# Kernel optimization log

Hardware: AMD Instinct MI355X
Metric: run time of the kernel (lower is better)

The kernel has to match this reference:

```python
import jax, jax.numpy as jnp
import numpy as np
import math

B = 16          # graphs per batch
N = 2048        # nodes per graph
F_IN = 64       # input node features
E_PER = 32768   # edges per graph
E = B * E_PER
H = 128         # hidden width (fixed by module)
C = 10          # output classes
K = math.ceil(0.8 * N)  # TopKPooling keep count per graph = 1639


def setup_inputs() -> dict:
    key = jax.random.key(0)
    ks = jax.random.split(key, 24)
    x = jax.random.normal(ks[0], (B * N, F_IN), jnp.float32)
    # intra-graph random edges (source->target), global node ids
    gid = jnp.repeat(jnp.arange(B, dtype=jnp.int32), E_PER)
    src = gid * N + jax.random.randint(ks[1], (E,), 0, N, dtype=jnp.int32)
    dst = gid * N + jax.random.randint(ks[2], (E,), 0, N, dtype=jnp.int32)

    def lin_w(k, o, i):
        return jax.random.normal(k, (o, i), jnp.float32) / jnp.sqrt(i)

    inp = dict(x=x, src=src, dst=dst)
    # GraphConv: lin_rel (with bias) on aggregated neighbors + lin_root (no bias)
    inp.update(W1_rel=lin_w(ks[3], H, F_IN), b1=jnp.zeros((H,), jnp.float32), W1_root=lin_w(ks[4], H, F_IN))
    inp.update(W2_rel=lin_w(ks[5], H, H), b2=jnp.zeros((H,), jnp.float32), W2_root=lin_w(ks[6], H, H))
    inp.update(W3_rel=lin_w(ks[7], H, H), b3=jnp.zeros((H,), jnp.float32), W3_root=lin_w(ks[8], H, H))
    inp.update(pool_w=jax.random.normal(ks[9], (H,), jnp.float32) / jnp.sqrt(H))
    inp.update(Wl1=lin_w(ks[10], 128, 256), bl1=jnp.zeros((128,), jnp.float32))
    inp.update(Wl2=lin_w(ks[11], 64, 128), bl2=jnp.zeros((64,), jnp.float32))
    inp.update(Wl3=lin_w(ks[12], C, 64), bl3=jnp.zeros((C,), jnp.float32))
    return inp


def _graph_conv(x, src, dst, W_rel, b, W_root, n_nodes, emask=None):
    # out_i = W_rel @ (sum_{j->i} x_j) + b + W_root @ x_i
    msg = x[src]
    if emask is not None:
        msg = msg * emask[:, None]
    agg = jax.ops.segment_sum(msg, dst, num_segments=n_nodes)
    return agg @ W_rel.T + b + x @ W_root.T


def _global_pools(x, n_per_graph):
    xb = x.reshape(B, n_per_graph, -1)
    return jnp.concatenate([xb.max(axis=1), xb.mean(axis=1)], axis=1)  # [B, 2F]


def reference(x, src, dst, W1_rel, b1, W1_root, W2_rel, b2, W2_root,
              W3_rel, b3, W3_root, pool_w, Wl1, bl1, Wl2, bl2, Wl3, bl3):
    n0 = B * N
    h = jax.nn.relu(_graph_conv(x, src, dst, W1_rel, b1, W1_root, n0))
    x1 = _global_pools(h, N)

    h = jax.nn.relu(_graph_conv(h, src, dst, W2_rel, b2, W2_root, n0))

    # TopKPooling(ratio=0.8): score = tanh(x@w/||w||); keep top-k per graph;
    # kept features scaled by score; edges with a dropped endpoint removed.
    score = jnp.tanh((h @ pool_w) / jnp.linalg.norm(pool_w))  # [B*N]
    top_s, top_i = jax.lax.top_k(score.reshape(B, N), K)      # [B,K]
    perm = (top_i + jnp.arange(B)[:, None] * N).reshape(-1)   # global old ids [B*K]
    h = h[perm] * top_s.reshape(-1)[:, None]                  # [B*K, H]

    n1 = B * K
    new_id = jnp.full((n0,), -1, jnp.int32).at[perm].set(jnp.arange(n1, dtype=jnp.int32))
    ns, nd = new_id[src], new_id[dst]
    keep = ((ns >= 0) & (nd >= 0)).astype(h.dtype)
    ns = jnp.where(ns >= 0, ns, 0)
    nd = jnp.where(nd >= 0, nd, 0)

    x2 = _global_pools(h, K)
    h = jax.nn.relu(_graph_conv(h, ns, nd, W3_rel, b3, W3_root, n1, emask=keep))
    x3 = _global_pools(h, K)

    z = x1 + x2 + x3
    z = jax.nn.relu(z @ Wl1.T + bl1)
    z = jax.nn.relu(z @ Wl2.T + bl2)
    return jax.nn.log_softmax(z @ Wl3.T + bl3, axis=-1)  # [B, C]
```

## Files before the change

kernel.cpp:

```cpp
#include <hip/hip_runtime.h>
#include <hip/hip_bf16.h>
#include <math.h>

#define NB 32768
#define NN 2048
#define BG 16
#define KK 1639
#define KKP 1664
#define N1 (BG*KK)
#define N1P (BG*KKP)
#define EE 524288
#define HH 128
#define FIN 64

using half8 = __attribute__((ext_vector_type(8))) _Float16;
using half4 = __attribute__((ext_vector_type(4))) _Float16;
using f32x4 = __attribute__((ext_vector_type(4))) float;

__device__ __forceinline__ void acc4(f32x4& a, const float4& v) {
  a[0] += v.x; a[1] += v.y; a[2] += v.z; a[3] += v.w;
}

__global__ void deg_kernel(const int* __restrict__ dst, int* deg, int n) {
  int e = blockIdx.x * blockDim.x + threadIdx.x;
  if (e < n) atomicAdd(&deg[dst[e]], 1);
}

__global__ void exscan_kernel(const int* __restrict__ deg, int* rs, int* cursor, int n) {
  __shared__ int wsum[16];
  __shared__ int carry;
  int t = threadIdx.x;
  int lane = t & 63, wid = t >> 6;
  if (t == 0) carry = 0;
  __syncthreads();
  int ntiles = (n + 4095) >> 12;
  for (int tile = 0; tile < ntiles; ++tile) {
    int idx = (tile << 12) + t * 4;
    int4 v4 = *(const int4*)(deg + idx);
    int v0 = (idx + 0 < n) ? v4.x : 0;
    int v1 = (idx + 1 < n) ? v4.y : 0;
    int v2 = (idx + 2 < n) ? v4.z : 0;
    int v3 = (idx + 3 < n) ? v4.w : 0;
    int s = v0 + v1 + v2 + v3;
    int pre = s;
#pragma unroll
    for (int off = 1; off < 64; off <<= 1) {
      int u = __shfl_up(pre, off, 64);
      if (lane >= off) pre += u;
    }
    if (lane == 63) wsum[wid] = pre;
    __syncthreads();
    int wbase = 0;
#pragma unroll
    for (int ww = 0; ww < 16; ++ww)
      if (ww < wid) wbase += wsum[ww];
    int ex = carry + wbase + (pre - s);
    int4 e4 = make_int4(ex, ex + v0, ex + v0 + v1, ex + v0 + v1 + v2);
    if (idx + 3 < n) {
      *(int4*)(rs + idx) = e4;
      *(int4*)(cursor + idx) = e4;
    } else {
      if (idx + 0 < n) { rs[idx + 0] = e4.x; cursor[idx + 0] = e4.x; }
      if (idx + 1 < n) { rs[idx + 1] = e4.y; cursor[idx + 1] = e4.y; }
      if (idx + 2 < n) { rs[idx + 2] = e4.z; cursor[idx + 2] = e4.z; }
    }
    int tot = 0;
    if (t == 1023) tot = ex + s;
    __syncthreads();
    if (t == 1023) carry = tot;
    __syncthreads();
  }
  if (t == 0) rs[n] = carry;
}

__global__ void scatter_kernel(const int* __restrict__ src, const int* __restrict__ dst,
                               int* cursor, int* csr, int n) {
  int e = blockIdx.x * blockDim.x + threadIdx.x;
  if (e < n) {
    int d = dst[e];
    int p = atomicAdd(&cursor[d], 1);
    csr[p] = src[e];
  }
}

template <int KD1, int KD2, int POOL, int SCORE, int REMAP>
__global__ __launch_bounds__(512, 4) void conv_mfma(
    const float* __restrict__ feat, const float* __restrict__ xr,
    const int* __restrict__ rs, const int* __restrict__ csr,
    const int* __restrict__ perm, const int* __restrict__ new_id,
    const _Float16* __restrict__ Wh, const _Float16* __restrict__ Wl,
    const float* __restrict__ bias, float* __restrict__ out, int M, int nwg,
    float* __restrict__ pmax, float* __restrict__ psum,
    const float* __restrict__ pw, float* __restrict__ score) {
  constexpr int KTOT = KD1 + KD2;
  constexpr int NSTEP = KTOT / 32;
  __shared__ _Float16 ah_lds[64 * KTOT];
  __shared__ _Float16 al_lds[64 * KTOT];
  __shared__ float sdot[64][8];
  __shared__ float swsq[8];

  int tid = threadIdx.x;
  int lane = tid & 63, wid = tid >> 6;
  int bq = nwg >> 3, br = nwg & 7, bx = blockIdx.x & 7, bi = blockIdx.x >> 3;
  int swz = (bx < br ? bx * (bq + 1) : br * (bq + 1) + (bx - br) * bq) + bi;
  int row0 = swz * 64;
  int ch0 = wid * 16;
  int col = lane & 15;
  int kseg = (lane >> 4) * 8;

  {
    constexpr int CH = KD1 / 4;
    constexpr int EPW = 64 / CH;
    int sub = lane / CH;
    int ch = lane % CH;
    const float4* feat4 = (const float4*)feat;
#pragma unroll
    for (int rr = 0; rr < 8; ++rr) {
      int gr = wid * 8 + rr;
      int grow = row0 + gr;
      int e0 = 0, e1 = 0;
      if (REMAP) {
        int g = grow / KKP, j = grow - g * KKP;
        if (j < KK) {
          int oldrow = perm[g * KK + j];
          e0 = rs[oldrow];
          e1 = rs[oldrow + 1];
        }
      } else {
        if (grow >= M) grow = M - 1;
        e0 = rs[grow];
        e1 = rs[grow + 1];
      }
      f32x4 a0 = {0.f, 0.f, 0.f, 0.f}, a1 = a0, a2 = a0, a3 = a0;
      int e = e0 + sub;
      for (; e + 7 * EPW < e1; e += 8 * EPW) {
        int c[8];
#pragma unroll
        for (int u = 0; u < 8; ++u) c[u] = csr[e + u * EPW];
        if (REMAP) {
#pragma unroll
          for (int u = 0; u < 8; ++u) c[u] = new_id[c[u]];
        }
        float4 v[8];
#pragma unroll
        for (int u = 0; u < 8; ++u) {
          int ci = (REMAP && c[u] < 0) ? 0 : c[u];
          v[u] = feat4[(size_t)ci * CH + ch];
        }
        if (REMAP) {
#pragma unroll
          for (int u = 0; u < 8; ++u)
            if (c[u] < 0) v[u] = make_float4(0.f, 0.f, 0.f, 0.f);
        }
        acc4(a0, v[0]); acc4(a1, v[1]); acc4(a2, v[2]); acc4(a3, v[3]);
        acc4(a0, v[4]); acc4(a1, v[5]); acc4(a2, v[6]); acc4(a3, v[7]);
      }
      for (; e + 3 * EPW < e1; e += 4 * EPW) {
        int c[4];
#pragma unroll
        for (int u = 0; u < 4; ++u) c[u] = csr[e + u * EPW];
        if (REMAP) {
#pragma unroll
          for (int u = 0; u < 4; ++u) c[u] = new_id[c[u]];
        }
        float4 v[4];
#pragma unroll
        for (int u = 0; u < 4; ++u) {
          int ci = (REMAP && c[u] < 0) ? 0 : c[u];
          v[u] = feat4[(size_t)ci * CH + ch];
        }
        if (REMAP) {
#pragma unroll
          for (int u = 0; u < 4; ++u)
            if (c[u] < 0) v[u] = make_float4(0.f, 0.f, 0.f, 0.f);
        }
        acc4(a0, v[0]); acc4(a1, v[1]); acc4(a2, v[2]); acc4(a3, v[3]);
      }
      for (; e < e1; e += EPW) {
        int c = csr[e];
        if (REMAP) {
          c = new_id[c];
          if (c < 0) continue;
        }
        float4 v = feat4[(size_t)c * CH + ch];
        acc4(a0, v);
      }
      f32x4 s = (a0 + a1) + (a2 + a3);
      if (EPW == 4) {
#pragma unroll
        for (int j = 0; j < 4; ++j) s[j] += __shfl_xor(s[j], 16, 64);
      }
      if (EPW >= 2) {
#pragma unroll
        for (int j = 0; j < 4; ++j) s[j] += __shfl_xor(s[j], 32, 64);
      }
      if (sub == 0) {
        half4 hi, lo;
#pragma unroll
        for (int j = 0; j < 4; ++j) {
          _Float16 h = (_Float16)s[j];
          hi[j] = h;
          lo[j] = (_Float16)(s[j] - (float)h);
        }
        int byte = ((gr * KTOT + ch * 4) * 2) ^ ((gr & 7) << 4);
        *(half4*)((char*)ah_lds + byte) = hi;
        *(half4*)((char*)al_lds + byte) = lo;
      }
    }
  }

  for (int idx = tid; idx < 64 * KD2 / 8; idx += 512) {
    int row = idx / (KD2 / 8);
    int kc = (idx % (KD2 / 8)) * 8;
    int grow = row0 + row;
    if (grow >= M) grow = M - 1;
    const float* sp = xr + (size_t)grow * KD2 + kc;
    float4 a0 = *(const float4*)sp;
    float4 a1 = *(const float4*)(sp + 4);
    float av[8] = {a0.x, a0.y, a0.z, a0.w, a1.x, a1.y, a1.z, a1.w};
    half8 vh, vl;
#pragma unroll
    for (int j = 0; j < 8; ++j) {
      _Float16 h = (_Float16)av[j];
      vh[j] = h;
      vl[j] = (_Float16)(av[j] - (float)h);
    }
    int byte = ((row * KTOT + KD1 + kc) * 2) ^ ((row & 7) << 4);
    *(half8*)((char*)ah_lds + byte) = vh;
    *(half8*)((char*)al_lds + byte) = vl;
  }

  size_t wbase = (size_t)(ch0 + col) * KTOT + kseg;
  half8 whc = *(const half8*)(Wh + wbase);
  half8 wlc = *(const half8*)(Wl + wbase);
  __syncthreads();

  f32x4 acc[4];
#pragma unroll
  for (int rf = 0; rf < 4; ++rf) acc[rf] = (f32x4){0.f, 0.f, 0.f, 0.f};
  int r = lane & 15;
#pragma unroll
  for (int s = 0; s < NSTEP; ++s) {
    half8 whn, wln;
    if (s + 1 < NSTEP) {
      whn = *(const half8*)(Wh + wbase + (s + 1) * 32);
      wln = *(const half8*)(Wl + wbase + (s + 1) * 32);
    }
#pragma unroll
    for (int rf = 0; rf < 4; ++rf) {
      int row = rf * 16 + r;
      int byte = ((row * KTOT + s * 32 + kseg) * 2) ^ ((row & 7) << 4);
      half8 a_h = *(const half8*)((const char*)ah_lds + byte);
      half8 a_l = *(const half8*)((const char*)al_lds + byte);
      acc[rf] = __builtin_amdgcn_mfma_f32_16x16x32_f16(a_l, whc, acc[rf], 0, 0, 0);
      acc[rf] = __builtin_amdgcn_mfma_f32_16x16x32_f16(a_h, wlc, acc[rf], 0, 0, 0);
      acc[rf] = __builtin_amdgcn_mfma_f32_16x16x32_f16(a_h, whc, acc[rf], 0, 0, 0);
    }
    if (s + 1 < NSTEP) { whc = whn; wlc = wln; }
  }

  float bv = bias[ch0 + col];
  float cmax = -3.402823466e38f, csum = 0.f;
  float wcol = SCORE ? pw[ch0 + col] : 0.f;
  float pd[4][4];
  int g = 0, rowbase = 0;
  if (POOL == 2) { g = row0 / KKP; rowbase = row0 - g * KKP; }
#pragma unroll
  for (int rf = 0; rf < 4; ++rf) {
    int orow0 = row0 + rf * 16 + (lane >> 4) * 4;
#pragma unroll
    for (int rr = 0; rr < 4; ++rr) {
      int orow = orow0 + rr;
      float v = fmaxf(acc[rf][rr] + bv, 0.f);
      if (orow < M) out[(size_t)orow * HH + ch0 + col] = v;
      if (POOL == 1) { cmax = fmaxf(cmax, v); csum += v; }
      if (POOL == 2) {
        int local = rowbase + rf * 16 + (lane >> 4) * 4 + rr;
        if (local < KK) { cmax = fmaxf(cmax, v); csum += v; }
      }
      if (SCORE) pd[rf][rr] = v * wcol;
    }
  }
  if (POOL) {
    cmax = fmaxf(cmax, __shfl_xor(cmax, 16, 64)); csum += __shfl_xor(csum, 16, 64);
    cmax = fmaxf(cmax, __shfl_xor(cmax, 32, 64)); csum += __shfl_xor(csum, 32, 64);
    if ((lane >> 4) == 0) {
      if (POOL == 1) {
        int gg = row0 >> 11, sb = (row0 & 2047) >> 6;
        pmax[(gg * 32 + sb) * HH + ch0 + col] = cmax;
        psum[(gg * 32 + sb) * HH + ch0 + col] = csum;
      } else {
        int sb = rowbase >> 6;
        pmax[(g * 26 + sb) * HH + ch0 + col] = cmax;
        psum[(g * 26 + sb) * HH + ch0 + col] = csum;
      }
    }
  }
  if (SCORE) {
#pragma unroll
    for (int rf = 0; rf < 4; ++rf)
#pragma unroll
      for (int rr = 0; rr < 4; ++rr) {
        float d = pd[rf][rr];
        d += __shfl_xor(d, 1, 64); d += __shfl_xor(d, 2, 64);
        d += __shfl_xor(d, 4, 64); d += __shfl_xor(d, 8, 64);
        if (col == 0) sdot[rf * 16 + (lane >> 4) * 4 + rr][wid] = d;
      }
    float wsq = wcol * wcol;
    wsq += __shfl_xor(wsq, 1, 64); wsq += __shfl_xor(wsq, 2, 64);
    wsq += __shfl_xor(wsq, 4, 64); wsq += __shfl_xor(wsq, 8, 64);
    if (lane == 0) swsq[wid] = wsq;
    __syncthreads();
    if (tid < 64) {
      float d = 0.f, q = 0.f;
#pragma unroll
      for (int wv = 0; wv < 8; ++wv) { d += sdot[tid][wv]; q += swsq[wv]; }
      score[row0 + tid] = tanhf(d * rsqrtf(q));
    }
  }
}

__global__ void prep_weights_f16(const float* __restrict__ W1_rel, const float* __restrict__ W1_root,
                                 const float* __restrict__ W2_rel, const float* __restrict__ W2_root,
                                 const float* __restrict__ W3_rel, const float* __restrict__ W3_root,
                                 _Float16* wh1, _Float16* wl1, _Float16* wh2, _Float16* wl2,
                                 _Float16* wh3, _Float16* wl3) {
  int idx = blockIdx.x * blockDim.x + threadIdx.x;
  float v;
  _Float16* ph;
  _Float16* pl;
  int j;
  if (idx < 128 * 128) {
    j = idx;
    int o = j >> 7, k = j & 127;
    v = (k < 64) ? W1_rel[o * 64 + k] : W1_root[o * 64 + (k - 64)];
    ph = wh1; pl = wl1;
  } else if (idx < 128 * 128 + 128 * 256) {
    j = idx - 128 * 128;
    int o = j >> 8, k = j & 255;
    v = (k < 128) ? W2_rel[o * 128 + k] : W2_root[o * 128 + (k - 128)];
    ph = wh2; pl = wl2;
  } else if (idx < 128 * 128 + 2 * 128 * 256) {
    j = idx - 128 * 128 - 128 * 256;
    int o = j >> 8, k = j & 255;
    v = (k < 128) ? W3_rel[o * 128 + k] : W3_root[o * 128 + (k - 128)];
    ph = wh3; pl = wl3;
  } else {
    return;
  }
  _Float16 h = (_Float16)v;
  ph[j] = h;
  pl[j] = (_Float16)(v - (float)h);
}

__global__ void topk_kernel(const float* __restrict__ score, int* perm) {
  __shared__ unsigned long long k[NN];
  int b = blockIdx.x;
  int tid = threadIdx.x;
  for (int i = tid; i < NN; i += 1024) {
    float s = score[b * NN + i];
    unsigned u = __float_as_uint(s);
    u = (u & 0x80000000u) ? ~u : (u | 0x80000000u);
    unsigned long long key = ((unsigned long long)u << 32) | (unsigned)(NN - 1 - i);
    k[i] = ~key;
  }
  __syncthreads();
  for (int kk = 2; kk <= NN; kk <<= 1) {
    for (int j = kk >> 1; j > 0; j >>= 1) {
      for (int t = tid; t < NN; t += 1024) {
        int ixj = t ^ j;
        if (ixj > t) {
          bool up = ((t & kk) == 0);
          unsigned long long a = k[t], c = k[ixj];
          if ((a > c) == up) { k[t] = c; k[ixj] = a; }
        }
      }
      __syncthreads();
    }
  }
  for (int j = tid; j < KK; j += 1024) {
    unsigned long long key = ~k[j];
    int i = (NN - 1) - (int)(key & 0xffffffffu);
    perm[b * KK + j] = b * NN + i;
  }
}

__global__ void h3_kernel(const float4* __restrict__ h2, const int* __restrict__ perm,
                          const float* __restrict__ score, float4* __restrict__ h3,
                          int* __restrict__ new_id) {
  int idx = blockIdx.x * blockDim.x + threadIdx.x;
  if (idx < N1 * 32) {
    int g = idx >> 5, c = idx & 31;
    int b = g / KK, j = g - b * KK;
    int p = perm[g];
    if (c == 0) new_id[p] = b * KKP + j;
    float s = score[p];
    float4 v = h2[(size_t)p * 32 + c];
    v.x *= s; v.y *= s; v.z *= s; v.w *= s;
    h3[(size_t)(b * KKP + j) * 32 + c] = v;
  }
}

__global__ void pool2_kernel(const float* __restrict__ h, float* pmax, float* psum) {
  int b = blockIdx.x / 26, s = blockIdx.x % 26;
  int f = threadIdx.x;
  int r0 = s * 64, r1 = min(KK, r0 + 64);
  float m = -3.402823466e38f, sum = 0.f;
  for (int r = r0; r < r1; ++r) {
    float v = h[(size_t)(b * KKP + r) * HH + f];
    m = fmaxf(m, v);
    sum += v;
  }
  pmax[(b * 26 + s) * HH + f] = m;
  psum[(b * 26 + s) * HH + f] = sum;
}

__global__ void mlp_kernel(const float* __restrict__ pm1, const float* __restrict__ ps1,
                           const float* __restrict__ pm2, const float* __restrict__ ps2,
                           const float* __restrict__ pm3, const float* __restrict__ ps3,
                           const float* __restrict__ Wl1, const float* __restrict__ bl1,
                           const float* __restrict__ Wl2, const float* __restrict__ bl2,
                           const float* __restrict__ Wl3, const float* __restrict__ bl3,
                           float* out) {
  __shared__ float z[256], a1[128], a2[64], a3[10], red[2];
  int b = blockIdx.x, t = threadIdx.x;
  float m1 = -3.402823466e38f, m2 = m1, m3 = m1;
  float s1 = 0.f, s2 = 0.f, s3 = 0.f;
  for (int s = 0; s < 32; ++s) {
    int o = (b * 32 + s) * 128 + t;
    m1 = fmaxf(m1, pm1[o]); s1 += ps1[o];
  }
  for (int s = 0; s < 26; ++s) {
    int o = (b * 26 + s) * 128 + t;
    m2 = fmaxf(m2, pm2[o]); s2 += ps2[o];
    m3 = fmaxf(m3, pm3[o]); s3 += ps3[o];
  }
  z[t] = m1 + m2 + m3;
  z[128 + t] = s1 * (1.f / NN) + (s2 + s3) * (1.f / KK);
  __syncthreads();
  {
    float acc = bl1[t];
    for (int q = 0; q < 256; ++q) acc = fmaf(Wl1[t * 256 + q], z[q], acc);
    a1[t] = fmaxf(acc, 0.f);
  }
  __syncthreads();
  if (t < 64) {
    float acc = bl2[t];
    for (int q = 0; q < 128; ++q) acc = fmaf(Wl2[t * 128 + q], a1[q], acc);
    a2[t] = fmaxf(acc, 0.f);
  }
  __syncthreads();
  if (t < 10) {
    float acc = bl3[t];
    for (int q = 0; q < 64; ++q) acc = fmaf(Wl3[t * 64 + q], a2[q], acc);
    a3[t] = acc;
  }
  __syncthreads();
  if (t == 0) {
    float m = a3[0];
    for (int i = 1; i < 10; ++i) m = fmaxf(m, a3[i]);
    float s = 0.f;
    for (int i = 0; i < 10; ++i) s += expf(a3[i] - m);
    red[0] = m;
    red[1] = logf(s);
  }
  __syncthreads();
  if (t < 10) out[b * 10 + t] = a3[t] - red[0] - red[1];
}

extern "C" void kernel_launch(void* const* d_in, const int* in_sizes, int n_in,
                              void* d_out, int out_size, void* d_ws, size_t ws_size,
                              hipStream_t stream) {
  const float* x       = (const float*)d_in[0];
  const int*   src     = (const int*)d_in[1];
  const int*   dst     = (const int*)d_in[2];
  const float* W1_rel  = (const float*)d_in[3];
  const float* b1      = (const float*)d_in[4];
  const float* W1_root = (const float*)d_in[5];
  const float* W2_rel  = (const float*)d_in[6];
  const float* b2      = (const float*)d_in[7];
  const float* W2_root = (const float*)d_in[8];
  const float* W3_rel  = (const float*)d_in[9];
  const float* b3      = (const float*)d_in[10];
  const float* W3_root = (const float*)d_in[11];
  const float* pool_w  = (const float*)d_in[12];
  const float* Wl1     = (const float*)d_in[13];
  const float* bl1     = (const float*)d_in[14];
  const float* Wl2     = (const float*)d_in[15];
  const float* bl2     = (const float*)d_in[16];
  const float* Wl3     = (const float*)d_in[17];
  const float* bl3     = (const float*)d_in[18];
  float* out = (float*)d_out;

  char* w = (char*)d_ws;
  size_t off = 0;
  auto alloc = [&](size_t bytes) -> char* {
    off = (off + 255) & ~(size_t)255;
    char* p = w + off;
    off += bytes;
    return p;
  };
  int* deg1     = (int*)alloc((NB + 4096) * 4);
  int* rs1      = (int*)alloc((NB + 1) * 4);
  int* cursor1  = (int*)alloc(NB * 4);
  int* csr1     = (int*)alloc((size_t)EE * 4);
  int* new_id   = (int*)alloc(NB * 4);
  int* perm     = (int*)alloc(N1 * 4);
  _Float16* wh1 = (_Float16*)alloc(128 * 128 * 2);
  _Float16* wl1 = (_Float16*)alloc(128 * 128 * 2);
  _Float16* wh2 = (_Float16*)alloc(128 * 256 * 2);
  _Float16* wl2 = (_Float16*)alloc(128 * 256 * 2);
  _Float16* wh3 = (_Float16*)alloc(128 * 256 * 2);
  _Float16* wl3 = (_Float16*)alloc(128 * 256 * 2);
  float* bufA   = (float*)alloc((size_t)NB * HH * 4);
  float* bufB   = (float*)alloc((size_t)NB * HH * 4);
  float* score  = (float*)alloc(NB * 4);
  float* pm1    = (float*)alloc(BG * 32 * HH * 4);
  float* ps1    = (float*)alloc(BG * 32 * HH * 4);
  float* pm2    = (float*)alloc(BG * 26 * HH * 4);
  float* ps2    = (float*)alloc(BG * 26 * HH * 4);
  float* pm3    = (float*)alloc(BG * 26 * HH * 4);
  float* ps3    = (float*)alloc(BG * 26 * HH * 4);
  if (off > ws_size) return;

  const int TB = 256;
  const int egrid = (EE + TB - 1) / TB;

  hipMemsetAsync(deg1, 0, (NB + 4096) * 4, stream);
  hipMemsetAsync(new_id, 0xFF, NB * 4, stream);

  prep_weights_f16<<<(128 * 128 + 2 * 128 * 256 + TB - 1) / TB, TB, 0, stream>>>(
      W1_rel, W1_root, W2_rel, W2_root, W3_rel, W3_root, wh1, wl1, wh2, wl2, wh3, wl3);

  deg_kernel<<<egrid, TB, 0, stream>>>(dst, deg1, EE);
  exscan_kernel<<<1, 1024, 0, stream>>>(deg1, rs1, cursor1, NB);
  scatter_kernel<<<egrid, TB, 0, stream>>>(src, dst, cursor1, csr1, EE);

  conv_mfma<64, 64, 1, 0, 0><<<NB / 64, 512, 0, stream>>>(
      x, x, rs1, csr1, nullptr, nullptr, wh1, wl1, b1, bufA, NB, NB / 64, pm1, ps1,
      nullptr, nullptr);

  conv_mfma<128, 128, 0, 1, 0><<<NB / 64, 512, 0, stream>>>(
      bufA, bufA, rs1, csr1, nullptr, nullptr, wh2, wl2, b2, bufB, NB, NB / 64,
      nullptr, nullptr, pool_w, score);

  topk_kernel<<<BG, 1024, 0, stream>>>(score, perm);
  h3_kernel<<<(N1 * 32 + TB - 1) / TB, TB, 0, stream>>>((const float4*)bufB, perm, score,
                                                        (float4*)bufA, new_id);
  pool2_kernel<<<BG * 26, 128, 0, stream>>>(bufA, pm2, ps2);

  conv_mfma<128, 128, 2, 0, 1><<<N1P / 64, 512, 0, stream>>>(
      bufA, bufA, rs1, csr1, perm, new_id, wh3, wl3, b3, bufB, N1P, N1P / 64, pm3, ps3,
      nullptr, nullptr);

  mlp_kernel<<<BG, 128, 0, stream>>>(pm1, ps1, pm2, ps2, pm3, ps3,
                                     Wl1, bl1, Wl2, bl2, Wl3, bl3, out);
}
```

Before: 239.0 us.

## Halve conv row tile to 32 and replace bitonic top-k with radix select

```diff
diff --git a/kernel.cpp b/kernel.cpp
--- a/kernel.cpp
+++ b/kernel.cpp
@@ -94,16 +94,16 @@
     const float* __restrict__ pw, float* __restrict__ score) {
   constexpr int KTOT = KD1 + KD2;
   constexpr int NSTEP = KTOT / 32;
-  __shared__ _Float16 ah_lds[64 * KTOT];
-  __shared__ _Float16 al_lds[64 * KTOT];
-  __shared__ float sdot[64][8];
+  __shared__ _Float16 ah_lds[32 * KTOT];
+  __shared__ _Float16 al_lds[32 * KTOT];
+  __shared__ float sdot[32][8];
   __shared__ float swsq[8];
 
   int tid = threadIdx.x;
   int lane = tid & 63, wid = tid >> 6;
   int bq = nwg >> 3, br = nwg & 7, bx = blockIdx.x & 7, bi = blockIdx.x >> 3;
   int swz = (bx < br ? bx * (bq + 1) : br * (bq + 1) + (bx - br) * bq) + bi;
-  int row0 = swz * 64;
+  int row0 = swz * 32;
   int ch0 = wid * 16;
   int col = lane & 15;
   int kseg = (lane >> 4) * 8;
@@ -115,8 +115,8 @@
     int ch = lane % CH;
     const float4* feat4 = (const float4*)feat;
 #pragma unroll
-    for (int rr = 0; rr < 8; ++rr) {
-      int gr = wid * 8 + rr;
+    for (int rr = 0; rr < 4; ++rr) {
+      int gr = wid * 4 + rr;
       int grow = row0 + gr;
       int e0 = 0, e1 = 0;
       if (REMAP) {
@@ -190,10 +190,8 @@
 #pragma unroll
         for (int j = 0; j < 4; ++j) s[j] += __shfl_xor(s[j], 16, 64);
       }
-      if (EPW >= 2) {
-#pragma unroll
-        for (int j = 0; j < 4; ++j) s[j] += __shfl_xor(s[j], 32, 64);
-      }
+#pragma unroll
+      for (int j = 0; j < 4; ++j) s[j] += __shfl_xor(s[j], 32, 64);
       if (sub == 0) {
         half4 hi, lo;
 #pragma unroll
@@ -209,7 +207,7 @@
     }
   }
 
-  for (int idx = tid; idx < 64 * KD2 / 8; idx += 512) {
+  for (int idx = tid; idx < 32 * KD2 / 8; idx += 512) {
     int row = idx / (KD2 / 8);
     int kc = (idx % (KD2 / 8)) * 8;
     int grow = row0 + row;
@@ -235,9 +233,9 @@
   half8 wlc = *(const half8*)(Wl + wbase);
   __syncthreads();
 
-  f32x4 acc[4];
-#pragma unroll
-  for (int rf = 0; rf < 4; ++rf) acc[rf] = (f32x4){0.f, 0.f, 0.f, 0.f};
+  f32x4 acc[2];
+#pragma unroll
+  for (int rf = 0; rf < 2; ++rf) acc[rf] = (f32x4){0.f, 0.f, 0.f, 0.f};
   int r = lane & 15;
 #pragma unroll
   for (int s = 0; s < NSTEP; ++s) {
@@ -247,7 +245,7 @@
       wln = *(const half8*)(Wl + wbase + (s + 1) * 32);
     }
 #pragma unroll
-    for (int rf = 0; rf < 4; ++rf) {
+    for (int rf = 0; rf < 2; ++rf) {
       int row = rf * 16 + r;
       int byte = ((row * KTOT + s * 32 + kseg) * 2) ^ ((row & 7) << 4);
       half8 a_h = *(const half8*)((const char*)ah_lds + byte);
@@ -262,11 +260,11 @@
   float bv = bias[ch0 + col];
   float cmax = -3.402823466e38f, csum = 0.f;
   float wcol = SCORE ? pw[ch0 + col] : 0.f;
-  float pd[4][4];
+  float pd[2][4];
   int g = 0, rowbase = 0;
   if (POOL == 2) { g = row0 / KKP; rowbase = row0 - g * KKP; }
 #pragma unroll
-  for (int rf = 0; rf < 4; ++rf) {
+  for (int rf = 0; rf < 2; ++rf) {
     int orow0 = row0 + rf * 16 + (lane >> 4) * 4;
 #pragma unroll
     for (int rr = 0; rr < 4; ++rr) {
@@ -286,19 +284,19 @@
     cmax = fmaxf(cmax, __shfl_xor(cmax, 32, 64)); csum += __shfl_xor(csum, 32, 64);
     if ((lane >> 4) == 0) {
       if (POOL == 1) {
-        int gg = row0 >> 11, sb = (row0 & 2047) >> 6;
-        pmax[(gg * 32 + sb) * HH + ch0 + col] = cmax;
-        psum[(gg * 32 + sb) * HH + ch0 + col] = csum;
+        int gg = row0 >> 11, sb = (row0 & 2047) >> 5;
+        pmax[(gg * 64 + sb) * HH + ch0 + col] = cmax;
+        psum[(gg * 64 + sb) * HH + ch0 + col] = csum;
       } else {
-        int sb = rowbase >> 6;
-        pmax[(g * 26 + sb) * HH + ch0 + col] = cmax;
-        psum[(g * 26 + sb) * HH + ch0 + col] = csum;
+        int sb = rowbase >> 5;
+        pmax[(g * 52 + sb) * HH + ch0 + col] = cmax;
+        psum[(g * 52 + sb) * HH + ch0 + col] = csum;
       }
     }
   }
   if (SCORE) {
 #pragma unroll
-    for (int rf = 0; rf < 4; ++rf)
+    for (int rf = 0; rf < 2; ++rf)
 #pragma unroll
       for (int rr = 0; rr < 4; ++rr) {
         float d = pd[rf][rr];
@@ -311,7 +309,7 @@
     wsq += __shfl_xor(wsq, 4, 64); wsq += __shfl_xor(wsq, 8, 64);
     if (lane == 0) swsq[wid] = wsq;
     __syncthreads();
-    if (tid < 64) {
+    if (tid < 32) {
       float d = 0.f, q = 0.f;
 #pragma unroll
       for (int wv = 0; wv < 8; ++wv) { d += sdot[tid][wv]; q += swsq[wv]; }
@@ -354,34 +352,65 @@
 }
 
 __global__ void topk_kernel(const float* __restrict__ score, int* perm) {
-  __shared__ unsigned long long k[NN];
-  int b = blockIdx.x;
-  int tid = threadIdx.x;
-  for (int i = tid; i < NN; i += 1024) {
+  __shared__ unsigned long long keys[NN];
+  __shared__ int hist[256];
+  __shared__ unsigned long long sP;
+  __shared__ int srem;
+  __shared__ int scnt;
+  int b = blockIdx.x, t = threadIdx.x;
+  for (int i = t; i < NN; i += 256) {
     float s = score[b * NN + i];
     unsigned u = __float_as_uint(s);
     u = (u & 0x80000000u) ? ~u : (u | 0x80000000u);
-    unsigned long long key = ((unsigned long long)u << 32) | (unsigned)(NN - 1 - i);
-    k[i] = ~key;
-  }
-  __syncthreads();
-  for (int kk = 2; kk <= NN; kk <<= 1) {
-    for (int j = kk >> 1; j > 0; j >>= 1) {
-      for (int t = tid; t < NN; t += 1024) {
-        int ixj = t ^ j;
-        if (ixj > t) {
-          bool up = ((t & kk) == 0);
-          unsigned long long a = k[t], c = k[ixj];
-          if ((a > c) == up) { k[t] = c; k[ixj] = a; }
-        }
-      }
-      __syncthreads();
-    }
-  }
-  for (int j = tid; j < KK; j += 1024) {
-    unsigned long long key = ~k[j];
-    int i = (NN - 1) - (int)(key & 0xffffffffu);
-    perm[b * KK + j] = b * NN + i;
+    keys[i] = ((unsigned long long)u << 32) | (unsigned)(NN - 1 - i);
+  }
+  if (t == 0) { sP = 0ULL; srem = KK; scnt = 0; }
+  __syncthreads();
+  for (int pass = 0; pass < 8; ++pass) {
+    int shift = 56 - 8 * pass;
+    for (int i = t; i < 256; i += 256) hist[i] = 0;
+    __syncthreads();
+    unsigned long long P = sP;
+    unsigned long long hm = (pass == 0) ? 0ULL : (~0ULL) << (shift + 8);
+    for (int i = t; i < NN; i += 256) {
+      unsigned long long k = keys[i];
+      if (((k ^ P) & hm) == 0) atomicAdd(&hist[(int)((k >> shift) & 255)], 1);
+    }
+    __syncthreads();
+    if (t < 64) {
+      int l = t;
+      int c[4], part = 0;
+#pragma unroll
+      for (int q = 0; q < 4; ++q) { c[q] = hist[255 - (l * 4 + q)]; part += c[q]; }
+      int pre = part;
+#pragma unroll
+      for (int off = 1; off < 64; off <<= 1) {
+        int u2 = __shfl_up(pre, off, 64);
+        if (l >= off) pre += u2;
+      }
+      int excl = pre - part;
+      int rem = srem;
+      if (excl < rem && rem <= excl + part) {
+        int run = excl;
+#pragma unroll
+        for (int q = 0; q < 4; ++q) {
+          if (run + c[q] >= rem) {
+            srem = rem - run;
+            sP = sP | ((unsigned long long)(255 - (l * 4 + q)) << shift);
+            break;
+          }
+          run += c[q];
+        }
+      }
+    }
+    __syncthreads();
+  }
+  unsigned long long T = sP;
+  for (int i = t; i < NN; i += 256) {
+    if (keys[i] >= T) {
+      int pos = atomicAdd(&scnt, 1);
+      perm[b * KK + pos] = b * NN + (NN - 1 - (int)(keys[i] & 0xffffffffULL));
+    }
   }
 }
 
@@ -426,13 +455,16 @@
   int b = blockIdx.x, t = threadIdx.x;
   float m1 = -3.402823466e38f, m2 = m1, m3 = m1;
   float s1 = 0.f, s2 = 0.f, s3 = 0.f;
-  for (int s = 0; s < 32; ++s) {
-    int o = (b * 32 + s) * 128 + t;
+  for (int s = 0; s < 64; ++s) {
+    int o = (b * 64 + s) * 128 + t;
     m1 = fmaxf(m1, pm1[o]); s1 += ps1[o];
   }
   for (int s = 0; s < 26; ++s) {
     int o = (b * 26 + s) * 128 + t;
     m2 = fmaxf(m2, pm2[o]); s2 += ps2[o];
+  }
+  for (int s = 0; s < 52; ++s) {
+    int o = (b * 52 + s) * 128 + t;
     m3 = fmaxf(m3, pm3[o]); s3 += ps3[o];
   }
   z[t] = m1 + m2 + m3;
@@ -515,12 +547,12 @@
   float* bufA   = (float*)alloc((size_t)NB * HH * 4);
   float* bufB   = (float*)alloc((size_t)NB * HH * 4);
   float* score  = (float*)alloc(NB * 4);
-  float* pm1    = (float*)alloc(BG * 32 * HH * 4);
-  float* ps1    = (float*)alloc(BG * 32 * HH * 4);
+  float* pm1    = (float*)alloc(BG * 64 * HH * 4);
+  float* ps1    = (float*)alloc(BG * 64 * HH * 4);
   float* pm2    = (float*)alloc(BG * 26 * HH * 4);
   float* ps2    = (float*)alloc(BG * 26 * HH * 4);
-  float* pm3    = (float*)alloc(BG * 26 * HH * 4);
-  float* ps3    = (float*)alloc(BG * 26 * HH * 4);
+  float* pm3    = (float*)alloc(BG * 52 * HH * 4);
+  float* ps3    = (float*)alloc(BG * 52 * HH * 4);
   if (off > ws_size) return;
 
   const int TB = 256;
@@ -536,21 +568,21 @@
   exscan_kernel<<<1, 1024, 0, stream>>>(deg1, rs1, cursor1, NB);
   scatter_kernel<<<egrid, TB, 0, stream>>>(src, dst, cursor1, csr1, EE);
 
-  conv_mfma<64, 64, 1, 0, 0><<<NB / 64, 512, 0, stream>>>(
-      x, x, rs1, csr1, nullptr, nullptr, wh1, wl1, b1, bufA, NB, NB / 64, pm1, ps1,
+  conv_mfma<64, 64, 1, 0, 0><<<NB / 32, 512, 0, stream>>>(
+      x, x, rs1, csr1, nullptr, nullptr, wh1, wl1, b1, bufA, NB, NB / 32, pm1, ps1,
       nullptr, nullptr);
 
-  conv_mfma<128, 128, 0, 1, 0><<<NB / 64, 512, 0, stream>>>(
-      bufA, bufA, rs1, csr1, nullptr, nullptr, wh2, wl2, b2, bufB, NB, NB / 64,
+  conv_mfma<128, 128, 0, 1, 0><<<NB / 32, 512, 0, stream>>>(
+      bufA, bufA, rs1, csr1, nullptr, nullptr, wh2, wl2, b2, bufB, NB, NB / 32,
       nullptr, nullptr, pool_w, score);
 
-  topk_kernel<<<BG, 1024, 0, stream>>>(score, perm);
+  topk_kernel<<<BG, 256, 0, stream>>>(score, perm);
   h3_kernel<<<(N1 * 32 + TB - 1) / TB, TB, 0, stream>>>((const float4*)bufB, perm, score,
                                                         (float4*)bufA, new_id);
   pool2_kernel<<<BG * 26, 128, 0, stream>>>(bufA, pm2, ps2);
 
-  conv_mfma<128, 128, 2, 0, 1><<<N1P / 64, 512, 0, stream>>>(
-      bufA, bufA, rs1, csr1, perm, new_id, wh3, wl3, b3, bufB, N1P, N1P / 64, pm3, ps3,
+  conv_mfma<128, 128, 2, 0, 1><<<N1P / 32, 512, 0, stream>>>(
+      bufA, bufA, rs1, csr1, perm, new_id, wh3, wl3, b3, bufB, N1P, N1P / 32, pm3, ps3,
       nullptr, nullptr);
 
   mlp_kernel<<<BG, 128, 0, stream>>>(pm1, ps1, pm2, ps2, pm3, ps3,
```

Result: slower. 255.4 us (+6.9%).
